# Kernel optimization log

Measured on AMD Instinct MI355X. Metric: run time of the kernel, lower is better.

## Reference

```python
import jax, jax.numpy as jnp
import numpy as np
import math

T, HW, M, D, DK, H, SIGMA = 16, 1024, 256, 768, 768, 8, 0.5
HD = DK // H
VHD = D // H
EPS = 1e-6
SCALE = 1.0 / math.sqrt(HD)


def _ln(x, g):
    # LayerNorm(eps=1e-6, bias=False)
    m = x.mean(-1, keepdims=True)
    v = ((x - m) ** 2).mean(-1, keepdims=True)
    return (x - m) / jnp.sqrt(v + EPS) * g


def setup_inputs() -> dict:
    key = jax.random.key(0)
    ks = jax.random.split(key, 16)
    s = 0.02
    features = jax.random.normal(ks[0], (T, HW, D), jnp.float32)
    tracks = jax.random.uniform(ks[1], (T, M, 2), jnp.float32)
    track_pos_embeddings = jax.random.normal(ks[2], (T, M, D), jnp.float32)
    feature_pos_embeddings = jax.random.normal(ks[3], (T, HW, D), jnp.float32)
    g = jnp.linspace(0.0, 1.0, 32)
    feature_positions = jnp.stack(jnp.meshgrid(g, g, indexing='ij'), axis=-1).reshape(HW, 2)
    return {
        'features': features,
        'tracks': tracks,
        'feature_positions': feature_positions,
        'track_pos_embeddings': track_pos_embeddings,
        'feature_pos_embeddings': feature_pos_embeddings,
        # AttentionalSampling params (nn.Linear weights are [out,in])
        'Wq_s': jax.random.normal(ks[4], (DK, D)) * s,
        'Wk_s': jax.random.normal(ks[5], (DK, D)) * s,
        'Wv_s': jax.random.normal(ks[6], (D, D)) * s,
        'qg_s': jnp.ones((DK,), jnp.float32),
        'kg_s': jnp.ones((DK,), jnp.float32),
        'Wo_s': jax.random.normal(ks[7], (D, D)) * s,
        # AttentionalSplatting params
        'Wq_p': jax.random.normal(ks[8], (DK, D)) * s,
        'Wk_p': jax.random.normal(ks[9], (DK, D)) * s,
        'Wv_p': jax.random.normal(ks[10], (D, D)) * s,
        'qg_p': jnp.ones((DK,), jnp.float32),
        'kg_p': jnp.ones((DK,), jnp.float32),
        'Wout_p': jax.random.normal(ks[11], (D, D)) * s,
    }


def reference(features, tracks, feature_positions, track_pos_embeddings,
              feature_pos_embeddings, Wq_s, Wk_s, Wv_s, qg_s, kg_s, Wo_s,
              Wq_p, Wk_p, Wv_p, qg_p, kg_p, Wout_p):
    # per-frame Gaussian spatial bias from squared euclidean distances
    # d2[t,m,n] = ||tracks[t,m] - feature_positions[n]||^2  -> [T, M, HW]
    d2 = ((tracks[:, :, None, :] - feature_positions[None, None, :, :]) ** 2).sum(-1)
    bias = -d2 / (2.0 * SIGMA ** 2)  # [T, M, HW]

    # ---- Attentional Sampling: tracks query features ----
    Q = _ln(track_pos_embeddings @ Wq_s.T, qg_s)          # [T, M, DK]
    K = _ln((features + feature_pos_embeddings) @ Wk_s.T, kg_s)  # [T, HW, DK]
    V = features @ Wv_s.T                                  # [T, HW, D]
    Qh = Q.reshape(T, M, H, HD).transpose(0, 2, 1, 3)      # [T, H, M, HD]
    Kh = K.reshape(T, HW, H, HD).transpose(0, 2, 1, 3)     # [T, H, HW, HD]
    Vh = V.reshape(T, HW, H, VHD).transpose(0, 2, 1, 3)    # [T, H, HW, VHD]
    scores = jnp.einsum('thmd,thnd->thmn', Qh, Kh) * SCALE + bias[:, None]
    A = jax.nn.softmax(scores, axis=-1)
    sampled = jnp.einsum('thmn,thnd->thmd', A, Vh)
    sampled = sampled.transpose(0, 2, 1, 3).reshape(T, M, D) @ Wo_s.T  # [T, M, D]

    # ---- Attentional Splatting: features query tracks ----
    Q2 = _ln(feature_pos_embeddings @ Wq_p.T, qg_p)        # [T, HW, DK]
    K2 = _ln(track_pos_embeddings @ Wk_p.T, kg_p)          # [T, M, DK]
    V2 = sampled @ Wv_p.T                                   # [T, M, D]
    Q2h = Q2.reshape(T, HW, H, HD).transpose(0, 2, 1, 3)   # [T, H, HW, HD]
    K2h = K2.reshape(T, M, H, HD).transpose(0, 2, 1, 3)    # [T, H, M, HD]
    V2h = V2.reshape(T, M, H, VHD).transpose(0, 2, 1, 3)   # [T, H, M, VHD]
    bias_t = jnp.swapaxes(bias, 1, 2)                       # [T, HW, M] (cdist is symmetric)
    scores2 = jnp.einsum('thnd,thmd->thnm', Q2h, K2h) * SCALE + bias_t[:, None]
    A2 = jax.nn.softmax(scores2, axis=-1)
    upd = jnp.einsum('thnm,thmd->thnd', A2, V2h)
    feature_updates = upd.transpose(0, 2, 1, 3).reshape(T, HW, D) @ Wout_p.T
    return features + feature_updates
```

## Files before the change

### kernel.cpp

```cpp
#include <hip/hip_runtime.h>

#define DD 768
#define HDIM 96
#define ATT_SCALE 0.10206207261596575f

typedef float floatx4 __attribute__((ext_vector_type(4)));
typedef __bf16 bf16;
typedef bf16 bf16x8 __attribute__((ext_vector_type(8)));
typedef bf16 bf16x4 __attribute__((ext_vector_type(4)));

__device__ __forceinline__ void gl2lds16(const bf16* g, bf16* l) {
  __builtin_amdgcn_global_load_lds(
      (const __attribute__((address_space(1))) void*)g,
      (__attribute__((address_space(3))) void*)l, 16, 0, 0);
}

__global__ __launch_bounds__(256) void conv_fuse(const float* __restrict__ f,
                                                 const float* __restrict__ e,
                                                 bf16* __restrict__ fb,
                                                 bf16* __restrict__ xb,
                                                 bf16* __restrict__ eb) {
  const int i = (blockIdx.x * 256 + threadIdx.x) * 8;
  floatx4 f0 = *(const floatx4*)(f + i);
  floatx4 f1 = *(const floatx4*)(f + i + 4);
  floatx4 e0 = *(const floatx4*)(e + i);
  floatx4 e1 = *(const floatx4*)(e + i + 4);
  bf16x8 fv, xv, ev;
#pragma unroll
  for (int k = 0; k < 4; k++) {
    fv[k] = (bf16)f0[k];           fv[k + 4] = (bf16)f1[k];
    ev[k] = (bf16)e0[k];           ev[k + 4] = (bf16)e1[k];
    xv[k] = (bf16)(f0[k] + e0[k]); xv[k + 4] = (bf16)(f1[k] + e1[k]);
  }
  *(bf16x8*)(fb + i) = fv;
  *(bf16x8*)(xb + i) = xv;
  *(bf16x8*)(eb + i) = ev;
}

__global__ __launch_bounds__(256) void f2b(const float* __restrict__ s,
                                           bf16* __restrict__ d) {
  const int i = (blockIdx.x * 256 + threadIdx.x) * 8;
  floatx4 s0 = *(const floatx4*)(s + i);
  floatx4 s1 = *(const floatx4*)(s + i + 4);
  bf16x8 v;
#pragma unroll
  for (int k = 0; k < 4; k++) { v[k] = (bf16)s0[k]; v[k + 4] = (bf16)s1[k]; }
  *(bf16x8*)(d + i) = v;
}

__global__ __launch_bounds__(256) void wconv(const float* w0, const float* w1,
                                             const float* w2, const float* w3,
                                             const float* w4, const float* w5,
                                             const float* w6, const float* w7,
                                             bf16* __restrict__ dst) {
  const float* srcs[8] = {w0, w1, w2, w3, w4, w5, w6, w7};
  const float* s = srcs[blockIdx.y];
  bf16* d = dst + (size_t)blockIdx.y * 589824;
  const int i = (blockIdx.x * 256 + threadIdx.x) * 8;
  floatx4 s0 = *(const floatx4*)(s + i);
  floatx4 s1 = *(const floatx4*)(s + i + 4);
  bf16x8 v;
#pragma unroll
  for (int k = 0; k < 4; k++) { v[k] = (bf16)s0[k]; v[k + 4] = (bf16)s1[k]; }
  *(bf16x8*)(d + i) = v;
}

__global__ __launch_bounds__(256) void ln_bf(bf16* __restrict__ X,
                                             const float* __restrict__ g) {
  const int w = threadIdx.x >> 6, lane = threadIdx.x & 63;
  bf16* x = X + (size_t)(blockIdx.x * 4 + w) * DD;
  float v[12], s = 0.f, ss = 0.f;
#pragma unroll
  for (int j = 0; j < 3; j++) {
    bf16x4 b = *(const bf16x4*)&x[j * 256 + lane * 4];
#pragma unroll
    for (int e = 0; e < 4; e++) {
      float t = (float)b[e];
      v[j * 4 + e] = t; s += t; ss += t * t;
    }
  }
#pragma unroll
  for (int o = 32; o > 0; o >>= 1) { s += __shfl_xor(s, o); ss += __shfl_xor(ss, o); }
  const float mean = s * (1.0f / DD);
  const float inv = rsqrtf(ss * (1.0f / DD) - mean * mean + 1e-6f);
#pragma unroll
  for (int j = 0; j < 3; j++) {
    floatx4 gg = *(const floatx4*)&g[j * 256 + lane * 4];
    bf16x4 o4;
#pragma unroll
    for (int e = 0; e < 4; e++) o4[e] = (bf16)((v[j * 4 + e] - mean) * inv * gg[e]);
    *(bf16x4*)&x[j * 256 + lane * 4] = o4;
  }
}

template <int MODE>
__global__ __launch_bounds__(256) void gemm128(const bf16* __restrict__ A,
                                               const bf16* __restrict__ W,
                                               bf16* __restrict__ Cb,
                                               float* __restrict__ Cf,
                                               const float* __restrict__ addsrc) {
  __shared__ bf16 As[128 * 32];
  __shared__ bf16 Ws[128 * 32];
  const int tid = threadIdx.x;
  const int lane = tid & 63;
  const int w = tid >> 6;
  const int row0 = blockIdx.x * 128;
  const int col0 = blockIdx.y * 128;
  const int wm = (w & 1) * 64;
  const int wn = (w >> 1) * 64;
  const int fr = lane & 15;
  const int quad = lane >> 4;
  const int srow = tid >> 2;
  const int scol = (tid & 3) * 8;
  const bf16* Ag = A + (size_t)(row0 + srow) * DD + scol;
  const bf16* Wg = W + (size_t)(col0 + srow) * DD + scol;
  bf16* AsD = &As[tid * 8];
  bf16* WsD = &Ws[tid * 8];

  floatx4 acc[4][4];
#pragma unroll
  for (int i = 0; i < 4; i++)
#pragma unroll
    for (int j = 0; j < 4; j++) acc[i][j] = (floatx4){0, 0, 0, 0};

  for (int k0 = 0; k0 < DD; k0 += 32) {
    __syncthreads();
    gl2lds16(Ag + k0, AsD);
    gl2lds16(Ag + k0 + (size_t)64 * DD, AsD + 2048);
    gl2lds16(Wg + k0, WsD);
    gl2lds16(Wg + k0 + (size_t)64 * DD, WsD + 2048);
    __syncthreads();
    bf16x8 af[4], bfr[4];
#pragma unroll
    for (int i = 0; i < 4; i++)
      af[i] = *(const bf16x8*)&As[(wm + i * 16 + fr) * 32 + quad * 8];
#pragma unroll
    for (int j = 0; j < 4; j++)
      bfr[j] = *(const bf16x8*)&Ws[(wn + j * 16 + fr) * 32 + quad * 8];
#pragma unroll
    for (int i = 0; i < 4; i++)
#pragma unroll
      for (int j = 0; j < 4; j++)
        acc[i][j] = __builtin_amdgcn_mfma_f32_16x16x32_bf16(af[i], bfr[j], acc[i][j], 0, 0, 0);
  }
#pragma unroll
  for (int i = 0; i < 4; i++)
#pragma unroll
    for (int j = 0; j < 4; j++)
#pragma unroll
      for (int r = 0; r < 4; r++) {
        const int row = row0 + wm + i * 16 + quad * 4 + r;
        const int col = col0 + wn + j * 16 + fr;
        const size_t idx = (size_t)row * DD + col;
        if (MODE == 0) Cb[idx] = (bf16)acc[i][j][r];
        else Cf[idx] = acc[i][j][r] + addsrc[idx];
      }
}

__global__ __launch_bounds__(256) void attn_kernel(
    const bf16* __restrict__ Qb, const bf16* __restrict__ Kb,
    const bf16* __restrict__ Vb, bf16* __restrict__ Ob,
    const float* __restrict__ qpos, int qpos_ts,
    const float* __restrict__ kpos, int kpos_ts,
    int nq, int nk) {
  const int t = blockIdx.z, h = blockIdx.y;
  const int q0 = blockIdx.x * 64;
  const bf16* Q = Qb + (size_t)t * nq * DD + h * HDIM;
  const bf16* K = Kb + (size_t)t * nk * DD + h * HDIM;
  const bf16* V = Vb + (size_t)t * nk * DD + h * HDIM;
  bf16* O = Ob + (size_t)t * nq * DD + h * HDIM;
  const float* qp = qpos + (size_t)t * qpos_ts;
  const float* kp = kpos + (size_t)t * kpos_ts;

  __shared__ bf16 Ks[64 * 104];
  __shared__ bf16 Vt[96 * 72];
  __shared__ bf16 Ps[64 * 72];

  const int tid = threadIdx.x;
  const int w = tid >> 6;
  const int lane = tid & 63;
  const int fr = lane & 15;
  const int quad = lane >> 4;

  bf16x8 qf[3];
  {
    const bf16* qrow = Q + (size_t)(q0 + w * 16 + fr) * DD;
#pragma unroll
    for (int c = 0; c < 3; c++) qf[c] = *(const bf16x8*)(qrow + c * 32 + quad * 8);
  }
  float qx[4], qy[4];
#pragma unroll
  for (int r = 0; r < 4; r++) {
    int qi = q0 + w * 16 + quad * 4 + r;
    qx[r] = qp[qi * 2];
    qy[r] = qp[qi * 2 + 1];
  }

  float mrow[4], lrow[4];
  floatx4 oacc[6];
#pragma unroll
  for (int r = 0; r < 4; r++) { mrow[r] = -1e30f; lrow[r] = 0.f; }
#pragma unroll
  for (int d = 0; d < 6; d++) oacc[d] = (floatx4){0, 0, 0, 0};

  const int srow = tid >> 2, scol = (tid & 3) * 24;
  const int vn = tid & 63, vd0 = (tid >> 6) * 24;

  for (int n0 = 0; n0 < nk; n0 += 64) {
    __syncthreads();
    {
      const bf16* kg = K + (size_t)(n0 + srow) * DD + scol;
      bf16* ks = &Ks[srow * 104 + scol];
#pragma unroll
      for (int c = 0; c < 3; c++) *(bf16x8*)(ks + c * 8) = *(const bf16x8*)(kg + c * 8);
    }
    {
      const bf16* vg = V + (size_t)(n0 + vn) * DD + vd0;
      bf16x8 v8[3];
#pragma unroll
      for (int c = 0; c < 3; c++) v8[c] = *(const bf16x8*)(vg + c * 8);
#pragma unroll
      for (int dd = 0; dd < 24; dd++) Vt[(vd0 + dd) * 72 + vn] = v8[dd >> 3][dd & 7];
    }
    __syncthreads();

    floatx4 s4[4];
#pragma unroll
    for (int j = 0; j < 4; j++) {
      floatx4 sa = {0, 0, 0, 0};
#pragma unroll
      for (int c = 0; c < 3; c++) {
        bf16x8 kf = *(const bf16x8*)&Ks[(j * 16 + fr) * 104 + c * 32 + quad * 8];
        sa = __builtin_amdgcn_mfma_f32_16x16x32_bf16(qf[c], kf, sa, 0, 0, 0);
      }
      s4[j] = sa;
    }
    float kxx[4], kyy[4];
#pragma unroll
    for (int j = 0; j < 4; j++) {
      int ki = (n0 + j * 16 + fr) * 2;
      kxx[j] = kp[ki];
      kyy[j] = kp[ki + 1];
    }
    float p[4][4], rmax[4], rsum[4], alpha[4];
#pragma unroll
    for (int r = 0; r < 4; r++) rmax[r] = -1e30f;
#pragma unroll
    for (int j = 0; j < 4; j++)
#pragma unroll
      for (int r = 0; r < 4; r++) {
        float dx = qx[r] - kxx[j], dy = qy[r] - kyy[j];
        float sv = s4[j][r] * ATT_SCALE - 2.0f * (dx * dx + dy * dy);
        p[j][r] = sv;
        rmax[r] = fmaxf(rmax[r], sv);
      }
#pragma unroll
    for (int r = 0; r < 4; r++) {
#pragma unroll
      for (int o = 1; o < 16; o <<= 1) rmax[r] = fmaxf(rmax[r], __shfl_xor(rmax[r], o));
      float mnew = fmaxf(mrow[r], rmax[r]);
      alpha[r] = __expf(mrow[r] - mnew);
      mrow[r] = mnew;
      rsum[r] = 0.f;
    }
#pragma unroll
    for (int j = 0; j < 4; j++)
#pragma unroll
      for (int r = 0; r < 4; r++) {
        float pv = __expf(p[j][r] - mrow[r]);
        p[j][r] = pv;
        rsum[r] += pv;
      }
#pragma unroll
    for (int r = 0; r < 4; r++) {
#pragma unroll
      for (int o = 1; o < 16; o <<= 1) rsum[r] += __shfl_xor(rsum[r], o);
      lrow[r] = lrow[r] * alpha[r] + rsum[r];
    }
#pragma unroll
    for (int j = 0; j < 4; j++)
#pragma unroll
      for (int r = 0; r < 4; r++)
        Ps[(w * 16 + quad * 4 + r) * 72 + j * 16 + fr] = (bf16)p[j][r];
#pragma unroll
    for (int d = 0; d < 6; d++)
#pragma unroll
      for (int r = 0; r < 4; r++) oacc[d][r] *= alpha[r];
    bf16x8 pf0 = *(const bf16x8*)&Ps[(w * 16 + fr) * 72 + quad * 8];
    bf16x8 pf1 = *(const bf16x8*)&Ps[(w * 16 + fr) * 72 + 32 + quad * 8];
#pragma unroll
    for (int d = 0; d < 6; d++) {
      bf16x8 v0 = *(const bf16x8*)&Vt[(d * 16 + fr) * 72 + quad * 8];
      bf16x8 v1 = *(const bf16x8*)&Vt[(d * 16 + fr) * 72 + 32 + quad * 8];
      oacc[d] = __builtin_amdgcn_mfma_f32_16x16x32_bf16(pf0, v0, oacc[d], 0, 0, 0);
      oacc[d] = __builtin_amdgcn_mfma_f32_16x16x32_bf16(pf1, v1, oacc[d], 0, 0, 0);
    }
  }
#pragma unroll
  for (int r = 0; r < 4; r++) {
    float inv = 1.0f / lrow[r];
    int row = q0 + w * 16 + quad * 4 + r;
#pragma unroll
    for (int d = 0; d < 6; d++)
      O[(size_t)row * DD + d * 16 + fr] = (bf16)(oacc[d][r] * inv);
  }
}

extern "C" void kernel_launch(void* const* d_in, const int* in_sizes, int n_in,
                              void* d_out, int out_size, void* d_ws, size_t ws_size,
                              hipStream_t stream) {
  const float* features = (const float*)d_in[0];
  const float* tracks   = (const float*)d_in[1];
  const float* fpos     = (const float*)d_in[2];
  const float* tpe      = (const float*)d_in[3];
  const float* fpe      = (const float*)d_in[4];
  const float* Wq_s     = (const float*)d_in[5];
  const float* Wk_s     = (const float*)d_in[6];
  const float* Wv_s     = (const float*)d_in[7];
  const float* qg_s     = (const float*)d_in[8];
  const float* kg_s     = (const float*)d_in[9];
  const float* Wo_s     = (const float*)d_in[10];
  const float* Wq_p     = (const float*)d_in[11];
  const float* Wk_p     = (const float*)d_in[12];
  const float* Wv_p     = (const float*)d_in[13];
  const float* qg_p     = (const float*)d_in[14];
  const float* kg_p     = (const float*)d_in[15];
  const float* Wout_p   = (const float*)d_in[16];
  float* out = (float*)d_out;

  const size_t SB = (size_t)16 * 1024 * 768;
  const size_t SS = (size_t)16 * 256 * 768;
  const size_t SW = (size_t)768 * 768;
  bf16* p = (bf16*)d_ws;
  bf16* Fb  = p; p += SB;
  bf16* Xb  = p; p += SB;
  bf16* Feb = p; p += SB;
  bf16* Kc  = p; p += SB;
  bf16* Vc  = p; p += SB;
  bf16* Tb  = p; p += SS;
  bf16* Qc  = p; p += SS;
  bf16* Sh  = p; p += SS;
  bf16* Sp  = p; p += SS;
  bf16* Wb  = p; p += 8 * SW;
  bf16* Q2 = Xb; bf16* K2 = Qc; bf16* V2 = Sh; bf16* U = Fb;

  dim3 blk(256);

  conv_fuse<<<6144, blk, 0, stream>>>(features, fpe, Fb, Xb, Feb);
  f2b<<<1536, blk, 0, stream>>>(tpe, Tb);
  wconv<<<dim3(288, 8), blk, 0, stream>>>(Wq_s, Wk_s, Wv_s, Wo_s,
                                          Wq_p, Wk_p, Wv_p, Wout_p, Wb);
  gemm128<0><<<dim3(128, 6), blk, 0, stream>>>(Xb, Wb + 1 * SW, Kc, nullptr, nullptr);
  ln_bf<<<4096, blk, 0, stream>>>(Kc, kg_s);
  gemm128<0><<<dim3(128, 6), blk, 0, stream>>>(Fb, Wb + 2 * SW, Vc, nullptr, nullptr);
  gemm128<0><<<dim3(32, 6), blk, 0, stream>>>(Tb, Wb + 0 * SW, Qc, nullptr, nullptr);
  ln_bf<<<1024, blk, 0, stream>>>(Qc, qg_s);
  attn_kernel<<<dim3(4, 8, 16), blk, 0, stream>>>(Qc, Kc, Vc, Sh,
                                                  tracks, 512, fpos, 0, 256, 1024);
  gemm128<0><<<dim3(32, 6), blk, 0, stream>>>(Sh, Wb + 3 * SW, Sp, nullptr, nullptr);
  gemm128<0><<<dim3(128, 6), blk, 0, stream>>>(Feb, Wb + 4 * SW, Q2, nullptr, nullptr);
  ln_bf<<<4096, blk, 0, stream>>>(Q2, qg_p);
  gemm128<0><<<dim3(32, 6), blk, 0, stream>>>(Tb, Wb + 5 * SW, K2, nullptr, nullptr);
  ln_bf<<<1024, blk, 0, stream>>>(K2, kg_p);
  gemm128<0><<<dim3(32, 6), blk, 0, stream>>>(Sp, Wb + 6 * SW, V2, nullptr, nullptr);
  attn_kernel<<<dim3(16, 8, 16), blk, 0, stream>>>(Q2, K2, V2, U,
                                                   fpos, 0, tracks, 512, 1024, 256);
  gemm128<1><<<dim3(128, 6), blk, 0, stream>>>(U, Wb + 7 * SW, nullptr, out, features);
}
```

Before: 531.5 us.

## Split-K attention for sampling, batch GEMMs and layernorms, multi-row attention tiles

Sampling attention over 1024 keys now splits keys across two blocks per query tile and writes partial outputs plus max/sum statistics. A new combine kernel merges them, so 1024 blocks run instead of 512. Independent GEMMs are batched into single launches via blockIdx.z, all four layernorms are fused into one launch, and the splatting attention processes two 16-row tiles per wave to reuse K/V loads. The V transpose into shared memory is restructured to use wider LDS stores. In exchange it adds a combine pass, extra workspace, and higher register pressure in the RPW=2 variant.

Result: no change. 539.9 us (+1.6%).

```diff
diff --git a/kernel.cpp b/kernel.cpp
--- a/kernel.cpp
+++ b/kernel.cpp
@@ -65,10 +65,7 @@
   *(bf16x8*)(d + i) = v;
 }
 
-__global__ __launch_bounds__(256) void ln_bf(bf16* __restrict__ X,
-                                             const float* __restrict__ g) {
-  const int w = threadIdx.x >> 6, lane = threadIdx.x & 63;
-  bf16* x = X + (size_t)(blockIdx.x * 4 + w) * DD;
+__device__ __forceinline__ void ln_row(bf16* x, const float* g, int lane) {
   float v[12], s = 0.f, ss = 0.f;
 #pragma unroll
   for (int j = 0; j < 3; j++) {
@@ -93,14 +90,27 @@
   }
 }
 
+__global__ __launch_bounds__(256) void ln_all(bf16* X0, const float* g0,
+                                              bf16* X1, const float* g1,
+                                              bf16* X2, const float* g2,
+                                              bf16* X3, const float* g3) {
+  const int b = blockIdx.x;
+  bf16* X; const float* g; int base;
+  if (b < 4096)      { X = X0; g = g0; base = b; }
+  else if (b < 8192) { X = X1; g = g1; base = b - 4096; }
+  else if (b < 9216) { X = X2; g = g2; base = b - 8192; }
+  else               { X = X3; g = g3; base = b - 9216; }
+  const int w = threadIdx.x >> 6, lane = threadIdx.x & 63;
+  ln_row(X + (size_t)(base * 4 + w) * DD, g, lane);
+}
+
 template <int MODE>
-__global__ __launch_bounds__(256) void gemm128(const bf16* __restrict__ A,
-                                               const bf16* __restrict__ W,
-                                               bf16* __restrict__ Cb,
-                                               float* __restrict__ Cf,
-                                               const float* __restrict__ addsrc) {
-  __shared__ bf16 As[128 * 32];
-  __shared__ bf16 Ws[128 * 32];
+__device__ __forceinline__ void gemm_core(const bf16* __restrict__ A,
+                                          const bf16* __restrict__ W,
+                                          bf16* __restrict__ Cb,
+                                          float* __restrict__ Cf,
+                                          const float* __restrict__ addsrc,
+                                          bf16* As, bf16* Ws) {
   const int tid = threadIdx.x;
   const int lane = tid & 63;
   const int w = tid >> 6;
@@ -157,56 +167,88 @@
       }
 }
 
+__global__ __launch_bounds__(256) void gemm_b(const bf16* A, const bf16* W, bf16* C) {
+  __shared__ bf16 As[4096], Ws[4096];
+  gemm_core<0>(A, W, C, nullptr, nullptr, As, Ws);
+}
+
+__global__ __launch_bounds__(256) void gemm_b2(const bf16* A0, const bf16* W0, bf16* C0,
+                                               const bf16* A1, const bf16* W1, bf16* C1) {
+  __shared__ bf16 As[4096], Ws[4096];
+  if (blockIdx.z == 0) gemm_core<0>(A0, W0, C0, nullptr, nullptr, As, Ws);
+  else                 gemm_core<0>(A1, W1, C1, nullptr, nullptr, As, Ws);
+}
+
+__global__ __launch_bounds__(256) void gemm_final(const bf16* A, const bf16* W,
+                                                  float* C, const float* addsrc) {
+  __shared__ bf16 As[4096], Ws[4096];
+  gemm_core<1>(A, W, nullptr, C, addsrc, As, Ws);
+}
+
+template <int RPW, int SPLIT>
 __global__ __launch_bounds__(256) void attn_kernel(
     const bf16* __restrict__ Qb, const bf16* __restrict__ Kb,
     const bf16* __restrict__ Vb, bf16* __restrict__ Ob,
+    float* __restrict__ Ml,
     const float* __restrict__ qpos, int qpos_ts,
     const float* __restrict__ kpos, int kpos_ts,
-    int nq, int nk) {
-  const int t = blockIdx.z, h = blockIdx.y;
-  const int q0 = blockIdx.x * 64;
+    int nq, int nk, int nqt, int nsp) {
+  const int b = blockIdx.x;
+  const int h = b & 7;
+  const int t = (b >> 3) & 15;
+  const int rest = b >> 7;
+  const int qt = rest % nqt;
+  const int sp = rest / nqt;
+  const int klen = nk / nsp;
+  const int k0s = sp * klen;
+  const int q0 = qt * (64 * RPW);
   const bf16* Q = Qb + (size_t)t * nq * DD + h * HDIM;
   const bf16* K = Kb + (size_t)t * nk * DD + h * HDIM;
   const bf16* V = Vb + (size_t)t * nk * DD + h * HDIM;
-  bf16* O = Ob + (size_t)t * nq * DD + h * HDIM;
+  bf16* O = Ob + (size_t)(SPLIT ? (sp * 16 + t) : t) * nq * DD + h * HDIM;
   const float* qp = qpos + (size_t)t * qpos_ts;
   const float* kp = kpos + (size_t)t * kpos_ts;
 
   __shared__ bf16 Ks[64 * 104];
   __shared__ bf16 Vt[96 * 72];
-  __shared__ bf16 Ps[64 * 72];
+  __shared__ bf16 Ps[RPW * 64 * 72];
 
   const int tid = threadIdx.x;
   const int w = tid >> 6;
   const int lane = tid & 63;
   const int fr = lane & 15;
   const int quad = lane >> 4;
-
-  bf16x8 qf[3];
-  {
-    const bf16* qrow = Q + (size_t)(q0 + w * 16 + fr) * DD;
-#pragma unroll
-    for (int c = 0; c < 3; c++) qf[c] = *(const bf16x8*)(qrow + c * 32 + quad * 8);
-  }
-  float qx[4], qy[4];
-#pragma unroll
-  for (int r = 0; r < 4; r++) {
-    int qi = q0 + w * 16 + quad * 4 + r;
-    qx[r] = qp[qi * 2];
-    qy[r] = qp[qi * 2 + 1];
-  }
-
-  float mrow[4], lrow[4];
-  floatx4 oacc[6];
-#pragma unroll
-  for (int r = 0; r < 4; r++) { mrow[r] = -1e30f; lrow[r] = 0.f; }
-#pragma unroll
-  for (int d = 0; d < 6; d++) oacc[d] = (floatx4){0, 0, 0, 0};
+  const int rowb = w * (16 * RPW);
+
+  bf16x8 qf[RPW][3];
+  float qx[RPW][4], qy[RPW][4];
+#pragma unroll
+  for (int rt = 0; rt < RPW; rt++) {
+    const bf16* qrow = Q + (size_t)(q0 + rowb + rt * 16 + fr) * DD;
+#pragma unroll
+    for (int c = 0; c < 3; c++) qf[rt][c] = *(const bf16x8*)(qrow + c * 32 + quad * 8);
+#pragma unroll
+    for (int r = 0; r < 4; r++) {
+      int qi = q0 + rowb + rt * 16 + quad * 4 + r;
+      qx[rt][r] = qp[qi * 2];
+      qy[rt][r] = qp[qi * 2 + 1];
+    }
+  }
+
+  float mrow[RPW][4], lrow[RPW][4];
+  floatx4 oacc[RPW][6];
+#pragma unroll
+  for (int rt = 0; rt < RPW; rt++) {
+#pragma unroll
+    for (int r = 0; r < 4; r++) { mrow[rt][r] = -1e30f; lrow[rt][r] = 0.f; }
+#pragma unroll
+    for (int d = 0; d < 6; d++) oacc[rt][d] = (floatx4){0, 0, 0, 0};
+  }
 
   const int srow = tid >> 2, scol = (tid & 3) * 24;
-  const int vn = tid & 63, vd0 = (tid >> 6) * 24;
-
-  for (int n0 = 0; n0 < nk; n0 += 64) {
+  const int nb = (tid & 15) * 4, db = (tid >> 4) * 6;
+
+  for (int n0 = k0s; n0 < k0s + klen; n0 += 64) {
     __syncthreads();
     {
       const bf16* kg = K + (size_t)(n0 + srow) * DD + scol;
@@ -215,26 +257,23 @@
       for (int c = 0; c < 3; c++) *(bf16x8*)(ks + c * 8) = *(const bf16x8*)(kg + c * 8);
     }
     {
-      const bf16* vg = V + (size_t)(n0 + vn) * DD + vd0;
-      bf16x8 v8[3];
-#pragma unroll
-      for (int c = 0; c < 3; c++) v8[c] = *(const bf16x8*)(vg + c * 8);
-#pragma unroll
-      for (int dd = 0; dd < 24; dd++) Vt[(vd0 + dd) * 72 + vn] = v8[dd >> 3][dd & 7];
+      bf16 tmp[4][6];
+#pragma unroll
+      for (int nn = 0; nn < 4; nn++) {
+        const unsigned* vg = (const unsigned*)(V + (size_t)(n0 + nb + nn) * DD + db);
+        unsigned u0 = vg[0], u1 = vg[1], u2 = vg[2];
+        *(unsigned*)&tmp[nn][0] = u0;
+        *(unsigned*)&tmp[nn][2] = u1;
+        *(unsigned*)&tmp[nn][4] = u2;
+      }
+#pragma unroll
+      for (int dd = 0; dd < 6; dd++) {
+        bf16x4 v4 = {tmp[0][dd], tmp[1][dd], tmp[2][dd], tmp[3][dd]};
+        *(bf16x4*)&Vt[(db + dd) * 72 + nb] = v4;
+      }
     }
     __syncthreads();
 
-    floatx4 s4[4];
-#pragma unroll
-    for (int j = 0; j < 4; j++) {
-      floatx4 sa = {0, 0, 0, 0};
-#pragma unroll
-      for (int c = 0; c < 3; c++) {
-        bf16x8 kf = *(const bf16x8*)&Ks[(j * 16 + fr) * 104 + c * 32 + quad * 8];
-        sa = __builtin_amdgcn_mfma_f32_16x16x32_bf16(qf[c], kf, sa, 0, 0, 0);
-      }
-      s4[j] = sa;
-    }
     float kxx[4], kyy[4];
 #pragma unroll
     for (int j = 0; j < 4; j++) {
@@ -242,67 +281,121 @@
       kxx[j] = kp[ki];
       kyy[j] = kp[ki + 1];
     }
-    float p[4][4], rmax[4], rsum[4], alpha[4];
-#pragma unroll
-    for (int r = 0; r < 4; r++) rmax[r] = -1e30f;
-#pragma unroll
-    for (int j = 0; j < 4; j++)
+
+#pragma unroll
+    for (int rt = 0; rt < RPW; rt++) {
+      floatx4 s4[4];
+#pragma unroll
+      for (int j = 0; j < 4; j++) {
+        floatx4 sa = {0, 0, 0, 0};
+#pragma unroll
+        for (int c = 0; c < 3; c++) {
+          bf16x8 kf = *(const bf16x8*)&Ks[(j * 16 + fr) * 104 + c * 32 + quad * 8];
+          sa = __builtin_amdgcn_mfma_f32_16x16x32_bf16(qf[rt][c], kf, sa, 0, 0, 0);
+        }
+        s4[j] = sa;
+      }
+      float p[4][4], rmax[4], rsum[4], alpha[4];
+#pragma unroll
+      for (int r = 0; r < 4; r++) rmax[r] = -1e30f;
+#pragma unroll
+      for (int j = 0; j < 4; j++)
+#pragma unroll
+        for (int r = 0; r < 4; r++) {
+          float dx = qx[rt][r] - kxx[j], dy = qy[rt][r] - kyy[j];
+          float sv = s4[j][r] * ATT_SCALE - 2.0f * (dx * dx + dy * dy);
+          p[j][r] = sv;
+          rmax[r] = fmaxf(rmax[r], sv);
+        }
 #pragma unroll
       for (int r = 0; r < 4; r++) {
-        float dx = qx[r] - kxx[j], dy = qy[r] - kyy[j];
-        float sv = s4[j][r] * ATT_SCALE - 2.0f * (dx * dx + dy * dy);
-        p[j][r] = sv;
-        rmax[r] = fmaxf(rmax[r], sv);
-      }
-#pragma unroll
-    for (int r = 0; r < 4; r++) {
-#pragma unroll
-      for (int o = 1; o < 16; o <<= 1) rmax[r] = fmaxf(rmax[r], __shfl_xor(rmax[r], o));
-      float mnew = fmaxf(mrow[r], rmax[r]);
-      alpha[r] = __expf(mrow[r] - mnew);
-      mrow[r] = mnew;
-      rsum[r] = 0.f;
-    }
-#pragma unroll
-    for (int j = 0; j < 4; j++)
+#pragma unroll
+        for (int o = 1; o < 16; o <<= 1) rmax[r] = fmaxf(rmax[r], __shfl_xor(rmax[r], o));
+        float mnew = fmaxf(mrow[rt][r], rmax[r]);
+        alpha[r] = __expf(mrow[rt][r] - mnew);
+        mrow[rt][r] = mnew;
+        rsum[r] = 0.f;
+      }
+#pragma unroll
+      for (int j = 0; j < 4; j++)
+#pragma unroll
+        for (int r = 0; r < 4; r++) {
+          float pv = __expf(p[j][r] - mrow[rt][r]);
+          p[j][r] = pv;
+          rsum[r] += pv;
+        }
 #pragma unroll
       for (int r = 0; r < 4; r++) {
-        float pv = __expf(p[j][r] - mrow[r]);
-        p[j][r] = pv;
-        rsum[r] += pv;
-      }
-#pragma unroll
-    for (int r = 0; r < 4; r++) {
-#pragma unroll
-      for (int o = 1; o < 16; o <<= 1) rsum[r] += __shfl_xor(rsum[r], o);
-      lrow[r] = lrow[r] * alpha[r] + rsum[r];
-    }
-#pragma unroll
-    for (int j = 0; j < 4; j++)
-#pragma unroll
-      for (int r = 0; r < 4; r++)
-        Ps[(w * 16 + quad * 4 + r) * 72 + j * 16 + fr] = (bf16)p[j][r];
-#pragma unroll
-    for (int d = 0; d < 6; d++)
-#pragma unroll
-      for (int r = 0; r < 4; r++) oacc[d][r] *= alpha[r];
-    bf16x8 pf0 = *(const bf16x8*)&Ps[(w * 16 + fr) * 72 + quad * 8];
-    bf16x8 pf1 = *(const bf16x8*)&Ps[(w * 16 + fr) * 72 + 32 + quad * 8];
+#pragma unroll
+        for (int o = 1; o < 16; o <<= 1) rsum[r] += __shfl_xor(rsum[r], o);
+        lrow[rt][r] = lrow[rt][r] * alpha[r] + rsum[r];
+      }
+#pragma unroll
+      for (int j = 0; j < 4; j++)
+#pragma unroll
+        for (int r = 0; r < 4; r++)
+          Ps[(rowb + rt * 16 + quad * 4 + r) * 72 + j * 16 + fr] = (bf16)p[j][r];
+#pragma unroll
+      for (int d = 0; d < 6; d++)
+#pragma unroll
+        for (int r = 0; r < 4; r++) oacc[rt][d][r] *= alpha[r];
+    }
+
+    bf16x8 pf[RPW][2];
+#pragma unroll
+    for (int rt = 0; rt < RPW; rt++) {
+      pf[rt][0] = *(const bf16x8*)&Ps[(rowb + rt * 16 + fr) * 72 + quad * 8];
+      pf[rt][1] = *(const bf16x8*)&Ps[(rowb + rt * 16 + fr) * 72 + 32 + quad * 8];
+    }
 #pragma unroll
     for (int d = 0; d < 6; d++) {
       bf16x8 v0 = *(const bf16x8*)&Vt[(d * 16 + fr) * 72 + quad * 8];
       bf16x8 v1 = *(const bf16x8*)&Vt[(d * 16 + fr) * 72 + 32 + quad * 8];
-      oacc[d] = __builtin_amdgcn_mfma_f32_16x16x32_bf16(pf0, v0, oacc[d], 0, 0, 0);
-      oacc[d] = __builtin_amdgcn_mfma_f32_16x16x32_bf16(pf1, v1, oacc[d], 0, 0, 0);
-    }
-  }
-#pragma unroll
-  for (int r = 0; r < 4; r++) {
-    float inv = 1.0f / lrow[r];
-    int row = q0 + w * 16 + quad * 4 + r;
-#pragma unroll
-    for (int d = 0; d < 6; d++)
-      O[(size_t)row * DD + d * 16 + fr] = (bf16)(oacc[d][r] * inv);
+#pragma unroll
+      for (int rt = 0; rt < RPW; rt++) {
+        oacc[rt][d] = __builtin_amdgcn_mfma_f32_16x16x32_bf16(pf[rt][0], v0, oacc[rt][d], 0, 0, 0);
+        oacc[rt][d] = __builtin_amdgcn_mfma_f32_16x16x32_bf16(pf[rt][1], v1, oacc[rt][d], 0, 0, 0);
+      }
+    }
+  }
+
+#pragma unroll
+  for (int rt = 0; rt < RPW; rt++)
+#pragma unroll
+    for (int r = 0; r < 4; r++) {
+      float inv = 1.0f / lrow[rt][r];
+      int row = q0 + rowb + rt * 16 + quad * 4 + r;
+#pragma unroll
+      for (int d = 0; d < 6; d++)
+        O[(size_t)row * DD + d * 16 + fr] = (bf16)(oacc[rt][d][r] * inv);
+      if (SPLIT && fr == 0) {
+        size_t mi = ((((size_t)sp * 16 + t) * 8 + h) * nq + row) * 2;
+        Ml[mi] = mrow[rt][r];
+        Ml[mi + 1] = lrow[rt][r];
+      }
+    }
+}
+
+__global__ __launch_bounds__(256) void combine2(const bf16* __restrict__ Op,
+                                                const float* __restrict__ Ml,
+                                                bf16* __restrict__ Out) {
+  const int row = blockIdx.x;
+  const int t = row >> 8;
+  const int q = row & 255;
+  const size_t half = (size_t)16 * 256 * DD;
+#pragma unroll
+  for (int e = 0; e < 3; e++) {
+    int dim = threadIdx.x + e * 256;
+    int hh = dim / 96;
+    size_t mi0 = (((size_t)t * 8 + hh) * 256 + q) * 2;
+    size_t mi1 = ((((size_t)16 + t) * 8 + hh) * 256 + q) * 2;
+    float m0 = Ml[mi0], l0 = Ml[mi0 + 1];
+    float m1 = Ml[mi1], l1 = Ml[mi1 + 1];
+    float mm = fmaxf(m0, m1);
+    float w0 = __expf(m0 - mm) * l0, w1 = __expf(m1 - mm) * l1;
+    float inv = 1.0f / (w0 + w1);
+    size_t idx = (size_t)row * DD + dim;
+    Out[idx] = (bf16)((w0 * (float)Op[idx] + w1 * (float)Op[idx + half]) * inv);
   }
 }
 
@@ -339,10 +432,13 @@
   bf16* Vc  = p; p += SB;
   bf16* Tb  = p; p += SS;
   bf16* Qc  = p; p += SS;
+  bf16* K2  = p; p += SS;
   bf16* Sh  = p; p += SS;
   bf16* Sp  = p; p += SS;
+  bf16* Op  = p; p += 2 * SS;
   bf16* Wb  = p; p += 8 * SW;
-  bf16* Q2 = Xb; bf16* K2 = Qc; bf16* V2 = Sh; bf16* U = Fb;
+  float* Ml = (float*)p;
+  bf16* Q2 = Xb; bf16* V2 = Sh; bf16* U = Fb;
 
   dim3 blk(256);
 
@@ -350,20 +446,18 @@
   f2b<<<1536, blk, 0, stream>>>(tpe, Tb);
   wconv<<<dim3(288, 8), blk, 0, stream>>>(Wq_s, Wk_s, Wv_s, Wo_s,
                                           Wq_p, Wk_p, Wv_p, Wout_p, Wb);
-  gemm128<0><<<dim3(128, 6), blk, 0, stream>>>(Xb, Wb + 1 * SW, Kc, nullptr, nullptr);
-  ln_bf<<<4096, blk, 0, stream>>>(Kc, kg_s);
-  gemm128<0><<<dim3(128, 6), blk, 0, stream>>>(Fb, Wb + 2 * SW, Vc, nullptr, nullptr);
-  gemm128<0><<<dim3(32, 6), blk, 0, stream>>>(Tb, Wb + 0 * SW, Qc, nullptr, nullptr);
-  ln_bf<<<1024, blk, 0, stream>>>(Qc, qg_s);
-  attn_kernel<<<dim3(4, 8, 16), blk, 0, stream>>>(Qc, Kc, Vc, Sh,
-                                                  tracks, 512, fpos, 0, 256, 1024);
-  gemm128<0><<<dim3(32, 6), blk, 0, stream>>>(Sh, Wb + 3 * SW, Sp, nullptr, nullptr);
-  gemm128<0><<<dim3(128, 6), blk, 0, stream>>>(Feb, Wb + 4 * SW, Q2, nullptr, nullptr);
-  ln_bf<<<4096, blk, 0, stream>>>(Q2, qg_p);
-  gemm128<0><<<dim3(32, 6), blk, 0, stream>>>(Tb, Wb + 5 * SW, K2, nullptr, nullptr);
-  ln_bf<<<1024, blk, 0, stream>>>(K2, kg_p);
-  gemm128<0><<<dim3(32, 6), blk, 0, stream>>>(Sp, Wb + 6 * SW, V2, nullptr, nullptr);
-  attn_kernel<<<dim3(16, 8, 16), blk, 0, stream>>>(Q2, K2, V2, U,
-                                                   fpos, 0, tracks, 512, 1024, 256);
-  gemm128<1><<<dim3(128, 6), blk, 0, stream>>>(U, Wb + 7 * SW, nullptr, out, features);
-}
+  gemm_b2<<<dim3(128, 6, 2), blk, 0, stream>>>(Xb, Wb + 1 * SW, Kc,
+                                               Fb, Wb + 2 * SW, Vc);
+  gemm_b<<<dim3(128, 6), blk, 0, stream>>>(Feb, Wb + 4 * SW, Q2);
+  gemm_b2<<<dim3(32, 6, 2), blk, 0, stream>>>(Tb, Wb + 0 * SW, Qc,
+                                              Tb, Wb + 5 * SW, K2);
+  ln_all<<<10240, blk, 0, stream>>>(Kc, kg_s, Q2, qg_p, Qc, qg_s, K2, kg_p);
+  attn_kernel<1, 1><<<1024, blk, 0, stream>>>(Qc, Kc, Vc, Op, Ml,
+                                              tracks, 512, fpos, 0, 256, 1024, 4, 2);
+  combine2<<<4096, blk, 0, stream>>>(Op, Ml, Sh);
+  gemm_b<<<dim3(32, 6), blk, 0, stream>>>(Sh, Wb + 3 * SW, Sp);
+  gemm_b<<<dim3(32, 6), blk, 0, stream>>>(Sp, Wb + 6 * SW, V2);
+  attn_kernel<2, 0><<<1024, blk, 0, stream>>>(Q2, K2, V2, U, nullptr,
+                                              fpos, 0, tracks, 512, 1024, 256, 8, 1);
+  gemm_final<<<dim3(128, 6), blk, 0, stream>>>(U, Wb + 7 * SW, out, features);
+}
```
